# Kernel tuning notes

Measured on AMD Instinct MI355X. Metric: run time of the kernel, lower is better.

Reference implementation:

```python
import jax, jax.numpy as jnp
import numpy as np

HEADS = 16
HEAD_DIM = 1024 // HEADS  # 64
SCALE = float(np.sqrt(HEAD_DIM))  # math.sqrt(features // heads)


def setup_inputs() -> dict:
    key = jax.random.key(0)
    ks = jax.random.split(key, 6)
    n, m, d, c = 2048, 2048, 1024, 768
    return {
        "x": jax.random.normal(ks[0], (n, d), dtype=jnp.float32),
        "ctx": jax.random.normal(ks[1], (m, c), dtype=jnp.float32),
        "Wq": jax.random.normal(ks[2], (d, d), dtype=jnp.float32) * (1.0 / np.sqrt(d)),
        "Wk": jax.random.normal(ks[3], (c, d), dtype=jnp.float32) * (1.0 / np.sqrt(c)),
        "Wv": jax.random.normal(ks[4], (c, d), dtype=jnp.float32) * (1.0 / np.sqrt(c)),
        "Wo": jax.random.normal(ks[5], (d, d), dtype=jnp.float32) * (1.0 / np.sqrt(d)),
    }


def reference(x, ctx, Wq, Wk, Wv, Wo):
    n, d = x.shape
    q = (x @ Wq).reshape(n, HEADS, HEAD_DIM).transpose(1, 0, 2)      # h n d
    k = (ctx @ Wk).reshape(-1, HEADS, HEAD_DIM).transpose(1, 0, 2)   # h m d
    v = (ctx @ Wv).reshape(-1, HEADS, HEAD_DIM).transpose(1, 0, 2)   # h m d
    scores = jnp.einsum("hnd,hmd->hnm", q, k) / SCALE
    attn = jax.nn.softmax(scores, axis=-1)
    out = jnp.einsum("hnm,hmd->hnd", attn, v)                        # h n d
    out = out.transpose(1, 0, 2).reshape(n, d)                       # n (h d)
    return out @ Wo
```

## Files before the change

kernel.cpp:

```cpp
#include <hip/hip_runtime.h>
#include <hip/hip_bf16.h>
#include <stdint.h>

typedef unsigned short bfu;
typedef __attribute__((ext_vector_type(8))) short short8;
typedef __attribute__((ext_vector_type(4))) float f32x4;

#define LOG2E 1.4426950408889634f

__device__ __forceinline__ bfu f2bf(float f) {
  union { float f; uint32_t u; } v; v.f = f;
  uint32_t r = (v.u + 0x7fffu + ((v.u >> 16) & 1u)) >> 16;
  return (bfu)r;
}

__device__ __forceinline__ void gload16(const void* g, void* l) {
  __builtin_amdgcn_global_load_lds((const __attribute__((address_space(1))) void*)g,
                                   (__attribute__((address_space(3))) void*)l, 16, 0, 0);
}

__device__ __forceinline__ void conv_body(const float* __restrict__ in, bfu* __restrict__ out,
                                          int i) {
  const float4* p = (const float4*)in + (size_t)i * 2;
  float4 a = p[0], b = p[1];
  union { bfu h[8]; uint4 v; } o;
  o.h[0] = f2bf(a.x); o.h[1] = f2bf(a.y); o.h[2] = f2bf(a.z); o.h[3] = f2bf(a.w);
  o.h[4] = f2bf(b.x); o.h[5] = f2bf(b.y); o.h[6] = f2bf(b.z); o.h[7] = f2bf(b.w);
  ((uint4*)out)[i] = o.v;
}

__device__ __forceinline__ void trans_body(const float* __restrict__ W, bfu* __restrict__ WT,
                                           int Kd, int n0, int k0) {
  __shared__ float tile[32][33];
  const int tx = threadIdx.x & 31, ty = threadIdx.x >> 5;
#pragma unroll
  for (int i = 0; i < 32; i += 8)
    tile[ty + i][tx] = W[(size_t)(k0 + ty + i) * 1024 + n0 + tx];
  __syncthreads();
#pragma unroll
  for (int i = 0; i < 32; i += 8)
    WT[(size_t)(n0 + ty + i) * Kd + k0 + tx] = f2bf(tile[tx][ty + i]);
}

__global__ __launch_bounds__(256) void prep_kernel(
    const float* __restrict__ x, const float* __restrict__ ctx,
    const float* __restrict__ Wq, const float* __restrict__ Wk,
    const float* __restrict__ Wv, const float* __restrict__ Wo,
    bfu* xb, bfu* ctxb, bfu* WTq, bfu* WTk, bfu* WTv, bfu* WTo) {
  int b = blockIdx.x;
  if (b < 1024)       conv_body(x, xb, b * 256 + threadIdx.x);
  else if (b < 1792)  conv_body(ctx, ctxb, (b - 1024) * 256 + threadIdx.x);
  else if (b < 2816) { b -= 1792; trans_body(Wq, WTq, 1024, (b & 31) * 32, (b >> 5) * 32); }
  else if (b < 3584) { b -= 2816; trans_body(Wk, WTk, 768, (b & 31) * 32, (b >> 5) * 32); }
  else if (b < 4352) { b -= 3584; trans_body(Wv, WTv, 768, (b & 31) * 32, (b >> 5) * 32); }
  else               { b -= 4352; trans_body(Wo, WTo, 1024, (b & 31) * 32, (b >> 5) * 32); }
}

typedef bfu Tile128[2][4][128][8];

__device__ __forceinline__ void gemm128_body(Tile128& As2, Tile128& Bs2,
    const bfu* __restrict__ A, const bfu* __restrict__ BT,
    bfu* __restrict__ Cb, int N, int K, float scale, int m0, int n0) {
  const int tid = threadIdx.x, lane = tid & 63, wave = tid >> 6;
  const int g = lane >> 4, c = lane & 15;
  const int wm = (wave >> 1) * 64, wn = (wave & 1) * 64;
  const int nt = K / 32;

  auto stage = [&](int buf, int kt) {
#pragma unroll
    for (int u = 0; u < 4; ++u) {
      int idx = wave * 4 + u;
      if (idx < 8) {
        int kg = idx & 3, rb = idx >> 2;
        gload16(&A[(size_t)(m0 + rb * 64 + lane) * K + kt + kg * 8], &As2[buf][kg][rb * 64][0]);
      } else {
        int kg = (idx - 8) & 3, rb = (idx - 8) >> 2;
        gload16(&BT[(size_t)(n0 + rb * 64 + lane) * K + kt + kg * 8], &Bs2[buf][kg][rb * 64][0]);
      }
    }
  };

  f32x4 acc[4][4] = {};
  stage(0, 0);
  for (int t = 0; t < nt; ++t) {
    __syncthreads();
    if (t + 1 < nt) stage((t + 1) & 1, (t + 1) * 32);
    const int b = t & 1;
    short8 af[4], bfr[4];
#pragma unroll
    for (int i = 0; i < 4; ++i) {
      af[i]  = *(const short8*)&As2[b][g][wm + i * 16 + c][0];
      bfr[i] = *(const short8*)&Bs2[b][g][wn + i * 16 + c][0];
    }
#pragma unroll
    for (int i = 0; i < 4; ++i)
#pragma unroll
      for (int j = 0; j < 4; ++j)
        acc[i][j] = __builtin_amdgcn_mfma_f32_16x16x32_bf16(af[i], bfr[j], acc[i][j], 0, 0, 0);
  }
#pragma unroll
  for (int i = 0; i < 4; ++i)
#pragma unroll
    for (int j = 0; j < 4; ++j) {
      int row = m0 + wm + i * 16 + g * 4;
      int col = n0 + wn + j * 16 + c;
#pragma unroll
      for (int r = 0; r < 4; ++r)
        Cb[(size_t)(row + r) * N + col] = f2bf(acc[i][j][r] * scale);
    }
}

typedef bfu AsArr[2][4][128][8];
typedef bfu BsArr[2][4][64][8];

__device__ __forceinline__ void gemm_body(AsArr& As2, BsArr& Bs2,
    const bfu* __restrict__ A, const bfu* __restrict__ BT,
    bfu* __restrict__ Cb, float* __restrict__ Cf,
    int N, int K, float scale, int m0, int n0) {
  const int tid = threadIdx.x, lane = tid & 63, wave = tid >> 6;
  const int g = lane >> 4, c = lane & 15;
  const int wm = wave * 32;
  const int nt = K / 32;

  auto stage = [&](int buf, int kt) {
#pragma unroll
    for (int u = 0; u < 3; ++u) {
      int idx = wave * 3 + u;
      if (idx < 8) {
        int g2 = idx & 3, rb = idx >> 2;
        gload16(&A[(size_t)(m0 + rb * 64 + lane) * K + kt + g2 * 8], &As2[buf][g2][rb * 64][0]);
      } else {
        int g2 = idx - 8;
        gload16(&BT[(size_t)(n0 + lane) * K + kt + g2 * 8], &Bs2[buf][g2][0][0]);
      }
    }
  };

  f32x4 acc[2][4] = {};
  stage(0, 0);
  for (int t = 0; t < nt; ++t) {
    __syncthreads();
    if (t + 1 < nt) stage((t + 1) & 1, (t + 1) * 32);
    const int b = t & 1;
    short8 af[2], bfr[4];
#pragma unroll
    for (int i = 0; i < 2; ++i) af[i] = *(const short8*)&As2[b][g][wm + i * 16 + c][0];
#pragma unroll
    for (int j = 0; j < 4; ++j) bfr[j] = *(const short8*)&Bs2[b][g][j * 16 + c][0];
#pragma unroll
    for (int i = 0; i < 2; ++i)
#pragma unroll
      for (int j = 0; j < 4; ++j)
        acc[i][j] = __builtin_amdgcn_mfma_f32_16x16x32_bf16(af[i], bfr[j], acc[i][j], 0, 0, 0);
  }
#pragma unroll
  for (int i = 0; i < 2; ++i)
#pragma unroll
    for (int j = 0; j < 4; ++j) {
      int row = m0 + wm + i * 16 + g * 4;
      int col = n0 + j * 16 + c;
#pragma unroll
      for (int r = 0; r < 4; ++r) {
        float v = acc[i][j][r] * scale;
        if (Cb) Cb[(size_t)(row + r) * N + col] = f2bf(v);
        else    Cf[(size_t)(row + r) * N + col] = v;
      }
    }
}

__global__ __launch_bounds__(256) void gemm3_kernel(
    const bfu* __restrict__ xb, const bfu* __restrict__ WTq, bfu* __restrict__ Qb,
    const bfu* __restrict__ ctxb, const bfu* __restrict__ WTk, bfu* __restrict__ Kb,
    const bfu* __restrict__ WTv, bfu* __restrict__ Vtb) {
  __shared__ alignas(16) bfu As2[2][4][128][8];
  __shared__ alignas(16) bfu Bs2[2][4][128][8];
  int bid = blockIdx.x;
  if (bid < 128)
    gemm128_body(As2, Bs2, xb, WTq, Qb, 1024, 1024, 0.125f * LOG2E, (bid >> 3) * 128, (bid & 7) * 128);
  else if (bid < 256) {
    int r = bid - 128;
    gemm128_body(As2, Bs2, ctxb, WTk, Kb, 1024, 768, 1.0f, (r >> 3) * 128, (r & 7) * 128);
  } else {
    int r = bid - 256;
    gemm_body(*(AsArr*)As2, *(BsArr*)Bs2, WTv, ctxb, Vtb, nullptr,
              2048, 768, 1.0f, (r >> 5) * 128, (r & 31) * 64);
  }
}

typedef bfu T64[2][4][64][8];

__global__ __launch_bounds__(128) void gemmo_kernel(const bfu* __restrict__ AO,
                                                    const bfu* __restrict__ WTo,
                                                    float* __restrict__ out) {
  __shared__ alignas(16) bfu As2[2][4][64][8];
  __shared__ alignas(16) bfu Bs2[2][4][64][8];
  const int tid = threadIdx.x, lane = tid & 63, wave = tid >> 6;
  const int g = lane >> 4, c = lane & 15;
  const int bid = blockIdx.x;
  const int xcd = bid & 7, slot = bid >> 3;
  const int m0 = (xcd * 4 + (slot >> 4)) * 64;
  const int n0 = (slot & 15) * 64;
  const int wm = wave * 32;
  const int K = 1024, N = 1024, nt = 32;

  auto stage = [&](int buf, int kt) {
#pragma unroll
    for (int u = 0; u < 4; ++u) {
      int idx = wave * 4 + u;
      if (idx < 4)
        gload16(&AO[(size_t)(m0 + lane) * K + kt + idx * 8], &As2[buf][idx][lane][0]);
      else
        gload16(&WTo[(size_t)(n0 + lane) * K + kt + (idx - 4) * 8], &Bs2[buf][idx - 4][lane][0]);
    }
  };

  f32x4 acc[2][4] = {};
  stage(0, 0);
  for (int t = 0; t < nt; ++t) {
    __syncthreads();
    if (t + 1 < nt) stage((t + 1) & 1, (t + 1) * 32);
    const int b = t & 1;
    short8 af[2], bfr[4];
#pragma unroll
    for (int i = 0; i < 2; ++i) af[i] = *(const short8*)&As2[b][g][wm + i * 16 + c][0];
#pragma unroll
    for (int j = 0; j < 4; ++j) bfr[j] = *(const short8*)&Bs2[b][g][j * 16 + c][0];
#pragma unroll
    for (int i = 0; i < 2; ++i)
#pragma unroll
      for (int j = 0; j < 4; ++j)
        acc[i][j] = __builtin_amdgcn_mfma_f32_16x16x32_bf16(af[i], bfr[j], acc[i][j], 0, 0, 0);
  }
#pragma unroll
  for (int i = 0; i < 2; ++i)
#pragma unroll
    for (int j = 0; j < 4; ++j) {
      int row = m0 + wm + i * 16 + g * 4;
      int col = n0 + j * 16 + c;
#pragma unroll
      for (int r = 0; r < 4; ++r)
        out[(size_t)(row + r) * N + col] = acc[i][j][r];
    }
}

__global__ __launch_bounds__(256) void attn_kernel(
    const bfu* __restrict__ Q, const bfu* __restrict__ Kmat,
    const bfu* __restrict__ Vt, bfu* __restrict__ O) {
  __shared__ alignas(16) bfu Ks[3][8][64][8];
  __shared__ alignas(16) bfu Vs[3][8][64][8];
  __shared__ alignas(16) bfu Ps[2][64][72];
  const int tid = threadIdx.x, wave = tid >> 6, lane = tid & 63;
  const int g = lane >> 4, c = lane & 15;
  const int bid = blockIdx.x;
  const int xcd = bid & 7, slot = bid >> 3;
  const int h = xcd + 8 * (slot >> 5);
  const int qblk = (slot & 31) * 64;
  const int col0 = h * 64;

  short8 qf[4][2];
#pragma unroll
  for (int qt = 0; qt < 4; ++qt) {
    qf[qt][0] = *(const short8*)&Q[(size_t)(qblk + qt * 16 + c) * 1024 + col0 + g * 8];
    qf[qt][1] = *(const short8*)&Q[(size_t)(qblk + qt * 16 + c) * 1024 + col0 + 32 + g * 8];
  }

  short8 ones;
#pragma unroll
  for (int e = 0; e < 8; ++e) ones[e] = (short)0x3F80;

  f32x4 o_acc[4] = {};
  f32x4 lacc = {};

  auto stage = [&](int buf, int kv0) {
#pragma unroll
    for (int u = 0; u < 4; ++u) {
      int idx = wave * 4 + u;
      if (idx < 8)
        gload16(&Kmat[(size_t)(kv0 + lane) * 1024 + col0 + idx * 8], &Ks[buf][idx][0][0]);
      else
        gload16(&Vt[(size_t)(col0 + lane) * 2048 + kv0 + (idx - 8) * 8], &Vs[buf][idx - 8][0][0]);
    }
  };

  auto qk_exp = [&](int bQ, int pb) {
    short8 kf0 = *(const short8*)&Ks[bQ][g][wave * 16 + c][0];
    short8 kf1 = *(const short8*)&Ks[bQ][4 + g][wave * 16 + c][0];
    f32x4 s[4] = {};
    __builtin_amdgcn_s_setprio(1);
#pragma unroll
    for (int qt = 0; qt < 4; ++qt) {
      s[qt] = __builtin_amdgcn_mfma_f32_16x16x32_bf16(qf[qt][0], kf0, s[qt], 0, 0, 0);
      s[qt] = __builtin_amdgcn_mfma_f32_16x16x32_bf16(qf[qt][1], kf1, s[qt], 0, 0, 0);
    }
    __builtin_amdgcn_s_setprio(0);
#pragma unroll
    for (int qt = 0; qt < 4; ++qt)
#pragma unroll
      for (int j = 0; j < 4; ++j)
        Ps[pb][qt * 16 + g * 4 + j][wave * 16 + c] =
            f2bf(__builtin_amdgcn_exp2f(s[qt][j]));
  };

  auto pv = [&](int pb, int vb) {
    __builtin_amdgcn_s_setprio(1);
#pragma unroll
    for (int kc = 0; kc < 2; ++kc) {
      short8 pf = *(const short8*)&Ps[pb][wave * 16 + c][kc * 32 + g * 8];
      lacc = __builtin_amdgcn_mfma_f32_16x16x32_bf16(pf, ones, lacc, 0, 0, 0);
#pragma unroll
      for (int fd = 0; fd < 4; ++fd) {
        short8 vf = *(const short8*)&Vs[vb][kc * 4 + g][fd * 16 + c][0];
        o_acc[fd] = __builtin_amdgcn_mfma_f32_16x16x32_bf16(pf, vf, o_acc[fd], 0, 0, 0);
      }
    }
    __builtin_amdgcn_s_setprio(0);
  };

  stage(0, 0);
  __syncthreads();
  stage(1, 64);
  qk_exp(0, 0);
  __syncthreads();
  for (int t = 1; t < 32; ++t) {
    stage((t + 1) % 3, ((t + 1) & 31) * 64);
    qk_exp(t % 3, t & 1);
    pv((t - 1) & 1, (t - 1) % 3);
    __syncthreads();
  }
  pv(1, 1);

  const int q0 = qblk + wave * 16;
#pragma unroll
  for (int fd = 0; fd < 4; ++fd)
#pragma unroll
    for (int j = 0; j < 4; ++j) {
      float v = o_acc[fd][j] / lacc[j];
      O[(size_t)(q0 + g * 4 + j) * 1024 + col0 + fd * 16 + c] = f2bf(v);
    }
}

extern "C" void kernel_launch(void* const* d_in, const int* in_sizes, int n_in,
                              void* d_out, int out_size, void* d_ws, size_t ws_size,
                              hipStream_t stream) {
  const float* x   = (const float*)d_in[0];
  const float* ctx = (const float*)d_in[1];
  const float* Wq  = (const float*)d_in[2];
  const float* Wk  = (const float*)d_in[3];
  const float* Wv  = (const float*)d_in[4];
  const float* Wo  = (const float*)d_in[5];
  float* out = (float*)d_out;

  bfu* ws   = (bfu*)d_ws;
  bfu* xb   = ws;
  bfu* WTk  = xb + 2048 * 1024;
  bfu* WTv  = WTk + 1024 * 768;
  bfu* WTo  = WTv + 1024 * 768;
  bfu* Qb   = WTo + 1024 * 1024;
  bfu* Kb   = Qb + 2048 * 1024;
  bfu* Vtb  = Kb + 2048 * 1024;
  bfu* WTq  = (bfu*)d_out;
  bfu* ctxb = WTq + 1024 * 1024;

  dim3 blk(256);
  prep_kernel<<<5376, blk, 0, stream>>>(x, ctx, Wq, Wk, Wv, Wo, xb, ctxb, WTq, WTk, WTv, WTo);
  gemm3_kernel<<<512, blk, 0, stream>>>(xb, WTq, Qb, ctxb, WTk, Kb, WTv, Vtb);
  attn_kernel<<<512, blk, 0, stream>>>(Qb, Kb, Vtb, xb);
  gemmo_kernel<<<512, dim3(128), 0, stream>>>(xb, WTo, out);
}
```

Before: 106.1 us.

## Split attention KV range across two blocks and merge partials in separate kernel

Attention now splits the 2048-long KV sequence into two halves handled by separate blocks (1024 blocks instead of 512), with KV tiles shrunk to 32 and each wave owning its own 16 query rows. The blocks write unnormalized fp32 partial outputs and row sums to workspace, and a new merge kernel adds the two halves, normalizes and converts to bf16. This aims to raise occupancy and parallelism in the attention stage. In exchange it adds fp32 partial-output traffic (about 16 MB written and read) and an extra kernel launch.

```diff
diff --git a/kernel.cpp b/kernel.cpp
--- a/kernel.cpp
+++ b/kernel.cpp
@@ -187,8 +187,6 @@
   }
 }
 
-typedef bfu T64[2][4][64][8];
-
 __global__ __launch_bounds__(128) void gemmo_kernel(const bfu* __restrict__ AO,
                                                     const bfu* __restrict__ WTo,
                                                     float* __restrict__ out) {
@@ -245,24 +243,23 @@
 
 __global__ __launch_bounds__(256) void attn_kernel(
     const bfu* __restrict__ Q, const bfu* __restrict__ Kmat,
-    const bfu* __restrict__ Vt, bfu* __restrict__ O) {
-  __shared__ alignas(16) bfu Ks[3][8][64][8];
-  __shared__ alignas(16) bfu Vs[3][8][64][8];
-  __shared__ alignas(16) bfu Ps[2][64][72];
+    const bfu* __restrict__ Vt, float* __restrict__ Opart, float* __restrict__ Lpart) {
+  __shared__ alignas(16) bfu Ks[3][8][32][8];
+  __shared__ alignas(16) bfu Vs[3][4][64][8];
+  __shared__ alignas(16) bfu Ps[2][64][40];
   const int tid = threadIdx.x, wave = tid >> 6, lane = tid & 63;
   const int g = lane >> 4, c = lane & 15;
   const int bid = blockIdx.x;
   const int xcd = bid & 7, slot = bid >> 3;
-  const int h = xcd + 8 * (slot >> 5);
-  const int qblk = (slot & 31) * 64;
+  const int h = xcd + 8 * (slot >> 6);
+  const int s2 = slot & 63;
+  const int qblk = (s2 >> 1) * 64;
+  const int half = s2 & 1;
+  const int kvbase = half * 1024;
   const int col0 = h * 64;
 
-  short8 qf[4][2];
-#pragma unroll
-  for (int qt = 0; qt < 4; ++qt) {
-    qf[qt][0] = *(const short8*)&Q[(size_t)(qblk + qt * 16 + c) * 1024 + col0 + g * 8];
-    qf[qt][1] = *(const short8*)&Q[(size_t)(qblk + qt * 16 + c) * 1024 + col0 + 32 + g * 8];
-  }
+  short8 qf0 = *(const short8*)&Q[(size_t)(qblk + wave * 16 + c) * 1024 + col0 + g * 8];
+  short8 qf1 = *(const short8*)&Q[(size_t)(qblk + wave * 16 + c) * 1024 + col0 + 32 + g * 8];
 
   short8 ones;
 #pragma unroll
@@ -273,56 +270,56 @@
 
   auto stage = [&](int buf, int kv0) {
 #pragma unroll
-    for (int u = 0; u < 4; ++u) {
-      int idx = wave * 4 + u;
-      if (idx < 8)
-        gload16(&Kmat[(size_t)(kv0 + lane) * 1024 + col0 + idx * 8], &Ks[buf][idx][0][0]);
-      else
-        gload16(&Vt[(size_t)(col0 + lane) * 2048 + kv0 + (idx - 8) * 8], &Vs[buf][idx - 8][0][0]);
+    for (int u = 0; u < 2; ++u) {
+      int idx = wave * 2 + u;
+      if (idx < 4) {
+        gload16(&Kmat[(size_t)(kv0 + (lane & 31)) * 1024 + col0 + (idx * 2 + (lane >> 5)) * 8],
+                &Ks[buf][idx * 2][0][0]);
+      } else {
+        int p = idx - 4;
+        gload16(&Vt[(size_t)(col0 + lane) * 2048 + kv0 + p * 8], &Vs[buf][p][0][0]);
+      }
     }
   };
 
   auto qk_exp = [&](int bQ, int pb) {
-    short8 kf0 = *(const short8*)&Ks[bQ][g][wave * 16 + c][0];
-    short8 kf1 = *(const short8*)&Ks[bQ][4 + g][wave * 16 + c][0];
-    f32x4 s[4] = {};
+    f32x4 s[2] = {};
     __builtin_amdgcn_s_setprio(1);
 #pragma unroll
-    for (int qt = 0; qt < 4; ++qt) {
-      s[qt] = __builtin_amdgcn_mfma_f32_16x16x32_bf16(qf[qt][0], kf0, s[qt], 0, 0, 0);
-      s[qt] = __builtin_amdgcn_mfma_f32_16x16x32_bf16(qf[qt][1], kf1, s[qt], 0, 0, 0);
+    for (int f = 0; f < 2; ++f) {
+      short8 kfa = *(const short8*)&Ks[bQ][g][f * 16 + c][0];
+      short8 kfb = *(const short8*)&Ks[bQ][4 + g][f * 16 + c][0];
+      s[f] = __builtin_amdgcn_mfma_f32_16x16x32_bf16(qf0, kfa, s[f], 0, 0, 0);
+      s[f] = __builtin_amdgcn_mfma_f32_16x16x32_bf16(qf1, kfb, s[f], 0, 0, 0);
     }
     __builtin_amdgcn_s_setprio(0);
 #pragma unroll
-    for (int qt = 0; qt < 4; ++qt)
+    for (int f = 0; f < 2; ++f)
 #pragma unroll
       for (int j = 0; j < 4; ++j)
-        Ps[pb][qt * 16 + g * 4 + j][wave * 16 + c] =
-            f2bf(__builtin_amdgcn_exp2f(s[qt][j]));
+        Ps[pb][wave * 16 + g * 4 + j][f * 16 + c] =
+            f2bf(__builtin_amdgcn_exp2f(s[f][j]));
   };
 
   auto pv = [&](int pb, int vb) {
     __builtin_amdgcn_s_setprio(1);
-#pragma unroll
-    for (int kc = 0; kc < 2; ++kc) {
-      short8 pf = *(const short8*)&Ps[pb][wave * 16 + c][kc * 32 + g * 8];
-      lacc = __builtin_amdgcn_mfma_f32_16x16x32_bf16(pf, ones, lacc, 0, 0, 0);
-#pragma unroll
-      for (int fd = 0; fd < 4; ++fd) {
-        short8 vf = *(const short8*)&Vs[vb][kc * 4 + g][fd * 16 + c][0];
-        o_acc[fd] = __builtin_amdgcn_mfma_f32_16x16x32_bf16(pf, vf, o_acc[fd], 0, 0, 0);
-      }
+    short8 pf = *(const short8*)&Ps[pb][wave * 16 + c][g * 8];
+    lacc = __builtin_amdgcn_mfma_f32_16x16x32_bf16(pf, ones, lacc, 0, 0, 0);
+#pragma unroll
+    for (int fd = 0; fd < 4; ++fd) {
+      short8 vf = *(const short8*)&Vs[vb][g][fd * 16 + c][0];
+      o_acc[fd] = __builtin_amdgcn_mfma_f32_16x16x32_bf16(pf, vf, o_acc[fd], 0, 0, 0);
     }
     __builtin_amdgcn_s_setprio(0);
   };
 
-  stage(0, 0);
+  stage(0, kvbase);
   __syncthreads();
-  stage(1, 64);
+  stage(1, kvbase + 32);
   qk_exp(0, 0);
   __syncthreads();
   for (int t = 1; t < 32; ++t) {
-    stage((t + 1) % 3, ((t + 1) & 31) * 64);
+    stage((t + 1) % 3, kvbase + ((t + 1) & 31) * 32);
     qk_exp(t % 3, t & 1);
     pv((t - 1) & 1, (t - 1) % 3);
     __syncthreads();
@@ -330,13 +327,34 @@
   pv(1, 1);
 
   const int q0 = qblk + wave * 16;
+  float* Op = Opart + (size_t)half * 2048 * 1024;
 #pragma unroll
   for (int fd = 0; fd < 4; ++fd)
 #pragma unroll
-    for (int j = 0; j < 4; ++j) {
-      float v = o_acc[fd][j] / lacc[j];
-      O[(size_t)(q0 + g * 4 + j) * 1024 + col0 + fd * 16 + c] = f2bf(v);
-    }
+    for (int j = 0; j < 4; ++j)
+      Op[(size_t)(q0 + g * 4 + j) * 1024 + col0 + fd * 16 + c] = o_acc[fd][j];
+  if (c == 0)
+#pragma unroll
+    for (int j = 0; j < 4; ++j)
+      Lpart[(half * 16 + h) * 2048 + q0 + g * 4 + j] = lacc[j];
+}
+
+__global__ __launch_bounds__(256) void merge_kernel(const float* __restrict__ Opart,
+                                                    const float* __restrict__ Lpart,
+                                                    bfu* __restrict__ xb) {
+  int idx4 = blockIdx.x * 256 + threadIdx.x;
+  int base = idx4 * 4;
+  int q = base >> 10, col = base & 1023, h = col >> 6;
+  float l = Lpart[h * 2048 + q] + Lpart[(16 + h) * 2048 + q];
+  float inv = 1.0f / l;
+  float4 a = ((const float4*)Opart)[idx4];
+  float4 b = ((const float4*)(Opart + 2048 * 1024))[idx4];
+  union { bfu h4[4]; ushort2 u2[2]; uint2 v; } o;
+  o.h4[0] = f2bf((a.x + b.x) * inv);
+  o.h4[1] = f2bf((a.y + b.y) * inv);
+  o.h4[2] = f2bf((a.z + b.z) * inv);
+  o.h4[3] = f2bf((a.w + b.w) * inv);
+  *(uint2*)&xb[base] = o.v;
 }
 
 extern "C" void kernel_launch(void* const* d_in, const int* in_sizes, int n_in,
@@ -358,12 +376,15 @@
   bfu* Qb   = WTo + 1024 * 1024;
   bfu* Kb   = Qb + 2048 * 1024;
   bfu* Vtb  = Kb + 2048 * 1024;
+  float* Opart = (float*)(Vtb + 2048 * 1024);
+  float* Lpart = Opart + 2 * 2048 * 1024;
   bfu* WTq  = (bfu*)d_out;
   bfu* ctxb = WTq + 1024 * 1024;
 
   dim3 blk(256);
   prep_kernel<<<5376, blk, 0, stream>>>(x, ctx, Wq, Wk, Wv, Wo, xb, ctxb, WTq, WTk, WTv, WTo);
   gemm3_kernel<<<512, blk, 0, stream>>>(xb, WTq, Qb, ctxb, WTk, Kb, WTv, Vtb);
-  attn_kernel<<<512, blk, 0, stream>>>(Qb, Kb, Vtb, xb);
+  attn_kernel<<<1024, blk, 0, stream>>>(Qb, Kb, Vtb, Opart, Lpart);
+  merge_kernel<<<2048, blk, 0, stream>>>(Opart, Lpart, xb);
   gemmo_kernel<<<512, dim3(128), 0, stream>>>(xb, WTo, out);
 }
```

Result: slower. 108.4 us (+2.1%).
